# Performance work log

Measured on AMD Instinct MI355X. Metric: run time of the kernel, lower is better.

## Reference

```python
import jax, jax.numpy as jnp
import numpy as np

# Winograd F(4x4, 5x5) transform matrices (input tile 8x8)
AT_NP = np.array([
    [1.0, 1.0, 1.0, 1.0, 1.0, 8.0, 8.0, 0.0],
    [0.0, 1.0, -1.0, 2.0, -2.0, 4.0, -4.0, 0.0],
    [0.0, 1.0, 1.0, 4.0, 4.0, 2.0, 2.0, 0.0],
    [0.0, 1.0, -1.0, 8.0, -8.0, 1.0, -1.0, 1.0]], dtype=np.float32)

BT_NP = np.array([
    [1.0, 0.0, -21.0/4.0, 0.0, 21.0/4.0, 0.0, -1.0, 0.0],
    [0.0, 1.0, 1.0, -17.0/4.0, -17.0/4.0, 1.0, 1.0, 0.0],
    [0.0, -1.0, 1.0, 17.0/4.0, -17.0/4.0, -1.0, 1.0, 0.0],
    [0.0, 0.5, 0.25, -2.5, -1.25, 2.0, 1.0, 0.0],
    [0.0, -0.5, 0.25, 2.5, -1.25, -2.0, 1.0, 0.0],
    [0.0, 2.0, 4.0, -2.5, -5.0, 0.5, 1.0, 0.0],
    [0.0, -2.0, 4.0, 2.5, -5.0, -0.5, 1.0, 0.0],
    [0.0, -1.0, 0.0, 21.0/4.0, 0.0, -21.0/4.0, 0.0, 1.0]], dtype=np.float32)

N, IC, OC, HW = 8, 128, 128, 68  # output spatial = 68-5+1 = 64, tiles 16x16


def setup_inputs() -> dict:
    key = jax.random.key(0)
    k1, k2, k3 = jax.random.split(key, 3)
    x = jax.random.normal(k1, (N, IC, HW, HW), dtype=jnp.float32)
    # weight is stored in the Winograd (transformed) domain: [OC, IC, 8, 8]
    weight = jax.random.normal(k2, (OC, IC, 8, 8), dtype=jnp.float32) * 0.02
    bias = 1.0 + 0.01 * jax.random.normal(k3, (OC,), dtype=jnp.float32)
    return {"x": x, "weight": weight, "bias": bias}


def reference(x, weight, bias):
    BT = jnp.asarray(BT_NP)
    AT = jnp.asarray(AT_NP)
    n, c, H, W = x.shape
    oc = weight.shape[0]
    tH = (H - 8) // 4 + 1
    tW = (W - 8) // 4 + 1
    # extract overlapping 8x8 tiles with stride 4 (torch unfold)
    ih = (jnp.arange(tH) * 4)[:, None] + jnp.arange(8)  # [tH, 8]
    iw = (jnp.arange(tW) * 4)[:, None] + jnp.arange(8)  # [tW, 8]
    tiles = x[:, :, ih, :]            # [n, c, tH, 8, W]
    tiles = tiles[:, :, :, :, iw]     # [n, c, tH, 8, tW, 8]
    tiles = tiles.transpose(0, 1, 2, 4, 3, 5)  # [n, c, tH, tW, 8, 8]
    # input transform: BT @ d @ B
    xt = jnp.einsum('ai,nchwij,bj->nchwab', BT, tiles, BT)
    # channel reduction with elementwise 8x8 multiply (Winograd domain)
    yt = jnp.einsum('nchwab,ocab->nohwab', xt, weight)
    # output transform: AT @ m @ A -> [n, oc, tH, tW, 4, 4]
    y = jnp.einsum('pa,nohwab,qb->nohwpq', AT, yt, AT)
    y = y.transpose(0, 1, 2, 4, 3, 5).reshape(n, oc, tH * 4, tW * 4)
    return y + bias[None, :, None, None]
```

## Files before the change

kernel.cpp:

```cpp
#include <hip/hip_runtime.h>

#define N_    8
#define IC_   128
#define OC_   128
#define HW_   68
#define M_    2048
#define OW_   64

constexpr float BT[8][8] = {
  {1.f, 0.f, -5.25f, 0.f, 5.25f, 0.f, -1.f, 0.f},
  {0.f, 1.f, 1.f, -4.25f, -4.25f, 1.f, 1.f, 0.f},
  {0.f, -1.f, 1.f, 4.25f, -4.25f, -1.f, 1.f, 0.f},
  {0.f, 0.5f, 0.25f, -2.5f, -1.25f, 2.f, 1.f, 0.f},
  {0.f, -0.5f, 0.25f, 2.5f, -1.25f, -2.f, 1.f, 0.f},
  {0.f, 2.f, 4.f, -2.5f, -5.f, 0.5f, 1.f, 0.f},
  {0.f, -2.f, 4.f, 2.5f, -5.f, -0.5f, 1.f, 0.f},
  {0.f, -1.f, 0.f, 5.25f, 0.f, -5.25f, 0.f, 1.f}
};
constexpr float AT[4][8] = {
  {1.f, 1.f, 1.f, 1.f, 1.f, 8.f, 8.f, 0.f},
  {0.f, 1.f, -1.f, 2.f, -2.f, 4.f, -4.f, 0.f},
  {0.f, 1.f, 1.f, 4.f, 4.f, 2.f, 2.f, 0.f},
  {0.f, 1.f, -1.f, 8.f, -8.f, 1.f, -1.f, 1.f}
};

__device__ __forceinline__ float bf2f(unsigned short u) {
  union { unsigned int i; float f; } v; v.i = ((unsigned int)u) << 16; return v.f;
}
__device__ __forceinline__ unsigned short f2bf(float f) {
  union { float f; unsigned int i; } v; v.f = f;
  unsigned int r = v.i + 0x7FFFu + ((v.i >> 16) & 1u);
  return (unsigned short)(r >> 16);
}

typedef __attribute__((ext_vector_type(8))) short short8;
typedef __attribute__((ext_vector_type(4))) float f32x4;

#define K1_CB 16
#define K1_PS 548
__global__ __launch_bounds__(256) void k_input_tf(const float* __restrict__ x,
                                                  unsigned short* __restrict__ xt) {
  const int cg = blockIdx.x, th = blockIdx.y, n = blockIdx.z;
  const int c0 = cg * K1_CB;
  const int h0 = th * 4;
  __shared__ float xs[K1_CB * K1_PS];

  const int tid = threadIdx.x;
  for (int idx = tid; idx < K1_CB * 8 * 17; idx += 256) {
    const int ci = idx / 136;
    const int rem = idx - ci * 136;
    const int r = rem / 17;
    const int f = rem - r * 17;
    const float4 v = *reinterpret_cast<const float4*>(
        x + ((size_t)((n * IC_ + c0 + ci) * HW_ + h0 + r)) * HW_ + f * 4);
    *reinterpret_cast<float4*>(&xs[ci * K1_PS + r * 68 + f * 4]) = v;
  }
  __syncthreads();

  const int cl = tid & 15;
  const int tw = tid >> 4;
  const float* xp = &xs[cl * K1_PS];

  float t1[8][8];
#pragma unroll
  for (int a = 0; a < 8; ++a)
#pragma unroll
    for (int j = 0; j < 8; ++j) t1[a][j] = 0.f;

#pragma unroll
  for (int i = 0; i < 8; ++i) {
    const float4 v0 = *reinterpret_cast<const float4*>(xp + i * 68 + tw * 4);
    const float4 v1 = *reinterpret_cast<const float4*>(xp + i * 68 + tw * 4 + 4);
    const float r[8] = {v0.x, v0.y, v0.z, v0.w, v1.x, v1.y, v1.z, v1.w};
#pragma unroll
    for (int a = 0; a < 8; ++a) {
      const float ba = BT[a][i];
      if (ba != 0.f) {
#pragma unroll
        for (int j = 0; j < 8; ++j) t1[a][j] += ba * r[j];
      }
    }
  }

  const int m = n * 256 + th * 16 + tw;
  const size_t base = (size_t)m * 128 + c0 + cl;
#pragma unroll
  for (int a = 0; a < 8; ++a) {
#pragma unroll
    for (int b = 0; b < 8; ++b) {
      float v = 0.f;
#pragma unroll
      for (int j = 0; j < 8; ++j) {
        const float bb = BT[b][j];
        if (bb != 0.f) v += t1[a][j] * bb;
      }
      xt[(size_t)(a * 8 + b) * (M_ * 128) + base] = f2bf(v);
    }
  }
}

__global__ __launch_bounds__(256) void k_wt(const float* __restrict__ w,
                                            unsigned short* __restrict__ wT) {
  const int idx = blockIdx.x * 256 + threadIdx.x;
  const int c  = idx & 127;
  const int oc = (idx >> 7) & 127;
  const int ab = idx >> 14;
  wT[idx] = f2bf(w[((size_t)oc * IC_ + c) * 64 + ab]);
}

__global__ __launch_bounds__(512) void k_gemm(const unsigned short* __restrict__ xt,
                                              const unsigned short* __restrict__ wT,
                                              unsigned short* __restrict__ yt) {
  const int ab = blockIdx.z;
  const int m0 = blockIdx.x * 128;
  const unsigned short* Ag = xt + (size_t)ab * (M_ * 128);
  const unsigned short* Bg = wT + (size_t)ab * (128 * 128);
  unsigned short* Cg = yt + (size_t)ab * (M_ * 128);

  __shared__ unsigned short As[128 * 128];
  __shared__ unsigned short Bs[128 * 128];

  const int tid = threadIdx.x;
  const int lane = tid & 63;
  const int wv = tid >> 6;

#pragma unroll
  for (int i = 0; i < 4; ++i) {
    const int inst = wv * 4 + i;
    const int r = inst * 4 + (lane >> 4);
    const int j = (lane & 15) ^ (r & 7);
    __builtin_amdgcn_global_load_lds(
        (const __attribute__((address_space(1))) void*)(Ag + (size_t)(m0 + r) * 128 + j * 8),
        (__attribute__((address_space(3))) void*)(As + inst * 512), 16, 0, 0);
  }
#pragma unroll
  for (int i = 0; i < 4; ++i) {
    const int inst = wv * 4 + i;
    const int r = inst * 4 + (lane >> 4);
    const int j = (lane & 15) ^ (r & 7);
    __builtin_amdgcn_global_load_lds(
        (const __attribute__((address_space(1))) void*)(Bg + (size_t)r * 128 + j * 8),
        (__attribute__((address_space(3))) void*)(Bs + inst * 512), 16, 0, 0);
  }
  __syncthreads();

  const int wm = wv >> 1, wn = wv & 1;
  const int m_base = wm * 32;
  const int oc_base = wn * 64;
  const int lr = lane & 15;
  const int lg = lane >> 4;

  f32x4 acc[2][4];
#pragma unroll
  for (int mi = 0; mi < 2; ++mi)
#pragma unroll
    for (int ni = 0; ni < 4; ++ni) acc[mi][ni] = (f32x4){0.f, 0.f, 0.f, 0.f};

#pragma unroll
  for (int kk = 0; kk < 4; ++kk) {
    short8 af[2], bf[4];
#pragma unroll
    for (int mi = 0; mi < 2; ++mi) {
      const int row = m_base + mi * 16 + lr;
      const int chunk = (kk * 4 + lg) ^ (row & 7);
      af[mi] = *reinterpret_cast<const short8*>(&As[row * 128 + chunk * 8]);
    }
#pragma unroll
    for (int ni = 0; ni < 4; ++ni) {
      const int row = oc_base + ni * 16 + lr;
      const int chunk = (kk * 4 + lg) ^ (row & 7);
      bf[ni] = *reinterpret_cast<const short8*>(&Bs[row * 128 + chunk * 8]);
    }
#pragma unroll
    for (int mi = 0; mi < 2; ++mi)
#pragma unroll
      for (int ni = 0; ni < 4; ++ni)
        acc[mi][ni] = __builtin_amdgcn_mfma_f32_16x16x32_bf16(af[mi], bf[ni], acc[mi][ni], 0, 0, 0);
  }

#pragma unroll
  for (int mi = 0; mi < 2; ++mi) {
#pragma unroll
    for (int ni = 0; ni < 4; ++ni) {
#pragma unroll
      for (int j = 0; j < 4; ++j) {
        const int row = m0 + m_base + mi * 16 + lg * 4 + j;
        const int col = oc_base + ni * 16 + lr;
        Cg[(size_t)row * 128 + col] = f2bf(acc[mi][ni][j]);
      }
    }
  }
}

#define K4_PS 260
__global__ __launch_bounds__(512) void k_output_tf(const unsigned short* __restrict__ yt,
                                                   const float* __restrict__ bias,
                                                   float* __restrict__ y) {
  const int og = blockIdx.x, th = blockIdx.y, n = blockIdx.z;
  const int oc0 = og * 32;
  const int tid = threadIdx.x;
  const int ocl = tid & 31;
  const int tw = tid >> 5;
  const int m = n * 256 + th * 16 + tw;

  __shared__ float ys[32 * K4_PS];

  float Y[8][8];
  const size_t rb = (size_t)m * 128 + oc0 + ocl;
#pragma unroll
  for (int a = 0; a < 8; ++a)
#pragma unroll
    for (int b = 0; b < 8; ++b)
      Y[a][b] = bf2f(yt[(size_t)(a * 8 + b) * (M_ * 128) + rb]);

  float t2[4][8];
#pragma unroll
  for (int p = 0; p < 4; ++p)
#pragma unroll
    for (int b = 0; b < 8; ++b) {
      float v = 0.f;
#pragma unroll
      for (int a = 0; a < 8; ++a) {
        const float aa = AT[p][a];
        if (aa != 0.f) v += aa * Y[a][b];
      }
      t2[p][b] = v;
    }

  const float bv = bias[oc0 + ocl];
#pragma unroll
  for (int p = 0; p < 4; ++p) {
    float o[4];
#pragma unroll
    for (int q = 0; q < 4; ++q) {
      float v = 0.f;
#pragma unroll
      for (int b = 0; b < 8; ++b) {
        const float ab_ = AT[q][b];
        if (ab_ != 0.f) v += t2[p][b] * ab_;
      }
      o[q] = v + bv;
    }
    const float4 ov = {o[0], o[1], o[2], o[3]};
    *reinterpret_cast<float4*>(&ys[ocl * K4_PS + p * 64 + tw * 4]) = ov;
  }
  __syncthreads();

#pragma unroll
  for (int it = 0; it < 4; ++it) {
    const int idx = it * 512 + tid;
    const int f = idx & 15;
    const int p = (idx >> 4) & 3;
    const int oo = idx >> 6;
    const float4 v = *reinterpret_cast<const float4*>(&ys[oo * K4_PS + p * 64 + f * 4]);
    *reinterpret_cast<float4*>(
        y + ((size_t)((n * OC_ + oc0 + oo) * OW_) + th * 4 + p) * OW_ + f * 4) = v;
  }
}

extern "C" void kernel_launch(void* const* d_in, const int* in_sizes, int n_in,
                              void* d_out, int out_size, void* d_ws, size_t ws_size,
                              hipStream_t stream) {
  (void)in_sizes; (void)n_in; (void)out_size; (void)ws_size;
  const float* x    = (const float*)d_in[0];
  const float* w    = (const float*)d_in[1];
  const float* bias = (const float*)d_in[2];
  float* y = (float*)d_out;

  char* ws = (char*)d_ws;
  unsigned short* xt = (unsigned short*)ws;
  unsigned short* yt = (unsigned short*)(ws + (size_t)32 * 1024 * 1024);
  unsigned short* wT = (unsigned short*)(ws + (size_t)64 * 1024 * 1024);

  hipLaunchKernelGGL(k_input_tf, dim3(8, 16, 8), dim3(256), 0, stream, x, xt);
  hipLaunchKernelGGL(k_wt, dim3((64 * 128 * 128) / 256), dim3(256), 0, stream, w, wT);
  hipLaunchKernelGGL(k_gemm, dim3(16, 1, 64), dim3(512), 0, stream, xt, wT, yt);
  hipLaunchKernelGGL(k_output_tf, dim3(4, 16, 8), dim3(512), 0, stream, yt, bias, y);
}
```

Before: 122.5 us.

## Fuse weight conversion into input transform, bf16 smem staging, retile output transform

Merges the weight bf16 transpose into the input-transform kernel as an extra grid row, which removes one kernel launch. The weight path now reads with float4 loads. The input transform uses 32 channels per block and stages x in shared memory as bf16 instead of fp32, halving LDS use. This rounds the input to bf16 before the Winograd transform, which adds precision error. The output transform now covers 64 output channels by 8 tiles per block and uses an XOR-swizzled shared layout to avoid bank conflicts, writing half-row 32-wide segments.

```diff
diff --git a/kernel.cpp b/kernel.cpp
--- a/kernel.cpp
+++ b/kernel.cpp
@@ -36,30 +36,51 @@
 typedef __attribute__((ext_vector_type(8))) short short8;
 typedef __attribute__((ext_vector_type(4))) float f32x4;
 
-#define K1_CB 16
-#define K1_PS 548
-__global__ __launch_bounds__(256) void k_input_tf(const float* __restrict__ x,
-                                                  unsigned short* __restrict__ xt) {
+#define K1_CPITCH 580
+__global__ __launch_bounds__(512) void k_in_wt(const float* __restrict__ x,
+                                               const float* __restrict__ w,
+                                               unsigned short* __restrict__ xt,
+                                               unsigned short* __restrict__ wT) {
   const int cg = blockIdx.x, th = blockIdx.y, n = blockIdx.z;
-  const int c0 = cg * K1_CB;
+  const int tid = threadIdx.x;
+
+  if (th == 16) {
+    const int wb = n * 4 + cg;
+    const int gtid = wb * 512 + tid;
+    for (int g = gtid; g < 262144; g += 16384) {
+      const int ab4 = g & 15;
+      const int c  = (g >> 4) & 127;
+      const int oc = g >> 11;
+      const float4 v = *reinterpret_cast<const float4*>(
+          w + ((size_t)(oc * 128 + c)) * 64 + ab4 * 4);
+      const float vv[4] = {v.x, v.y, v.z, v.w};
+#pragma unroll
+      for (int k = 0; k < 4; ++k)
+        wT[(size_t)(ab4 * 4 + k) * 16384 + oc * 128 + c] = f2bf(vv[k]);
+    }
+    return;
+  }
+
+  const int c0 = cg * 32;
   const int h0 = th * 4;
-  __shared__ float xs[K1_CB * K1_PS];
-
-  const int tid = threadIdx.x;
-  for (int idx = tid; idx < K1_CB * 8 * 17; idx += 256) {
+  __shared__ unsigned short xs[32 * K1_CPITCH];
+
+  for (int idx = tid; idx < 32 * 8 * 17; idx += 512) {
     const int ci = idx / 136;
     const int rem = idx - ci * 136;
     const int r = rem / 17;
     const int f = rem - r * 17;
     const float4 v = *reinterpret_cast<const float4*>(
         x + ((size_t)((n * IC_ + c0 + ci) * HW_ + h0 + r)) * HW_ + f * 4);
-    *reinterpret_cast<float4*>(&xs[ci * K1_PS + r * 68 + f * 4]) = v;
+    ushort4 s;
+    s.x = f2bf(v.x); s.y = f2bf(v.y); s.z = f2bf(v.z); s.w = f2bf(v.w);
+    *reinterpret_cast<ushort4*>(&xs[ci * K1_CPITCH + r * 72 + f * 4]) = s;
   }
   __syncthreads();
 
-  const int cl = tid & 15;
-  const int tw = tid >> 4;
-  const float* xp = &xs[cl * K1_PS];
+  const int ct = tid & 31;
+  const int tw = tid >> 5;
+  const unsigned short* xp = &xs[ct * K1_CPITCH];
 
   float t1[8][8];
 #pragma unroll
@@ -69,21 +90,22 @@
 
 #pragma unroll
   for (int i = 0; i < 8; ++i) {
-    const float4 v0 = *reinterpret_cast<const float4*>(xp + i * 68 + tw * 4);
-    const float4 v1 = *reinterpret_cast<const float4*>(xp + i * 68 + tw * 4 + 4);
-    const float r[8] = {v0.x, v0.y, v0.z, v0.w, v1.x, v1.y, v1.z, v1.w};
+    const ushort4 u0 = *reinterpret_cast<const ushort4*>(xp + i * 72 + tw * 4);
+    const ushort4 u1 = *reinterpret_cast<const ushort4*>(xp + i * 72 + tw * 4 + 4);
+    const float r8[8] = {bf2f(u0.x), bf2f(u0.y), bf2f(u0.z), bf2f(u0.w),
+                         bf2f(u1.x), bf2f(u1.y), bf2f(u1.z), bf2f(u1.w)};
 #pragma unroll
     for (int a = 0; a < 8; ++a) {
       const float ba = BT[a][i];
       if (ba != 0.f) {
 #pragma unroll
-        for (int j = 0; j < 8; ++j) t1[a][j] += ba * r[j];
+        for (int j = 0; j < 8; ++j) t1[a][j] += ba * r8[j];
       }
     }
   }
 
   const int m = n * 256 + th * 16 + tw;
-  const size_t base = (size_t)m * 128 + c0 + cl;
+  const size_t base = (size_t)m * 128 + c0 + ct;
 #pragma unroll
   for (int a = 0; a < 8; ++a) {
 #pragma unroll
@@ -97,15 +119,6 @@
       xt[(size_t)(a * 8 + b) * (M_ * 128) + base] = f2bf(v);
     }
   }
-}
-
-__global__ __launch_bounds__(256) void k_wt(const float* __restrict__ w,
-                                            unsigned short* __restrict__ wT) {
-  const int idx = blockIdx.x * 256 + threadIdx.x;
-  const int c  = idx & 127;
-  const int oc = (idx >> 7) & 127;
-  const int ab = idx >> 14;
-  wT[idx] = f2bf(w[((size_t)oc * IC_ + c) * 64 + ab]);
 }
 
 __global__ __launch_bounds__(512) void k_gemm(const unsigned short* __restrict__ xt,
@@ -192,18 +205,21 @@
   }
 }
 
-#define K4_PS 260
 __global__ __launch_bounds__(512) void k_output_tf(const unsigned short* __restrict__ yt,
                                                    const float* __restrict__ bias,
                                                    float* __restrict__ y) {
-  const int og = blockIdx.x, th = blockIdx.y, n = blockIdx.z;
-  const int oc0 = og * 32;
+  const int og = blockIdx.x;
+  const int thw = blockIdx.y;
+  const int n = blockIdx.z;
+  const int oc0 = og * 64;
   const int tid = threadIdx.x;
-  const int ocl = tid & 31;
-  const int tw = tid >> 5;
-  const int m = n * 256 + th * 16 + tw;
-
-  __shared__ float ys[32 * K4_PS];
+  const int ocl = tid & 63;
+  const int tw = tid >> 6;
+  const int m = n * 256 + thw * 8 + tw;
+  const int th = thw >> 1;
+  const int wq = thw & 1;
+
+  __shared__ float ys[64 * 128];
 
   float Y[8][8];
   const size_t rb = (size_t)m * 128 + oc0 + ocl;
@@ -242,19 +258,20 @@
       o[q] = v + bv;
     }
     const float4 ov = {o[0], o[1], o[2], o[3]};
-    *reinterpret_cast<float4*>(&ys[ocl * K4_PS + p * 64 + tw * 4]) = ov;
+    *reinterpret_cast<float4*>(&ys[ocl * 128 + p * 32 + ((tw ^ (ocl & 7)) * 4)]) = ov;
   }
   __syncthreads();
 
 #pragma unroll
   for (int it = 0; it < 4; ++it) {
     const int idx = it * 512 + tid;
-    const int f = idx & 15;
-    const int p = (idx >> 4) & 3;
-    const int oo = idx >> 6;
-    const float4 v = *reinterpret_cast<const float4*>(&ys[oo * K4_PS + p * 64 + f * 4]);
+    const int f = idx & 7;
+    const int p = (idx >> 3) & 3;
+    const int row = idx >> 5;
+    const float4 v = *reinterpret_cast<const float4*>(
+        &ys[row * 128 + p * 32 + ((f ^ (row & 7)) * 4)]);
     *reinterpret_cast<float4*>(
-        y + ((size_t)((n * OC_ + oc0 + oo) * OW_) + th * 4 + p) * OW_ + f * 4) = v;
+        y + (((size_t)(n * OC_ + oc0 + row) * OW_) + th * 4 + p) * OW_ + wq * 32 + f * 4) = v;
   }
 }
 
@@ -272,8 +289,7 @@
   unsigned short* yt = (unsigned short*)(ws + (size_t)32 * 1024 * 1024);
   unsigned short* wT = (unsigned short*)(ws + (size_t)64 * 1024 * 1024);
 
-  hipLaunchKernelGGL(k_input_tf, dim3(8, 16, 8), dim3(256), 0, stream, x, xt);
-  hipLaunchKernelGGL(k_wt, dim3((64 * 128 * 128) / 256), dim3(256), 0, stream, w, wT);
+  hipLaunchKernelGGL(k_in_wt, dim3(4, 17, 8), dim3(512), 0, stream, x, w, xt, wT);
   hipLaunchKernelGGL(k_gemm, dim3(16, 1, 64), dim3(512), 0, stream, xt, wT, yt);
-  hipLaunchKernelGGL(k_output_tf, dim3(4, 16, 8), dim3(512), 0, stream, yt, bias, y);
-}
+  hipLaunchKernelGGL(k_output_tf, dim3(2, 32, 8), dim3(512), 0, stream, yt, bias, y);
+}
```

After: 119.7 us. 2.3% less time.
